# Optimization experiments

Measured on AMD Instinct MI355X. Metric: run time of the kernel, lower is better.

The kernel has to match this reference:

```python
import jax, jax.numpy as jnp
import numpy as np

# Dims (match init_kwargs)
T = 1024      # num_tokens
H = 1024      # hidden_size
F = 768       # inter_size (ffn dim)
E = 16        # expert_num
K = 4         # moe_k


def setup_inputs() -> dict:
    key = jax.random.key(0)
    k1, k2, k3, k4 = jax.random.split(key, 4)
    hidden_states = jax.random.normal(k1, (T, H), dtype=jnp.float32)
    gate_w = jax.random.normal(k2, (E, H), dtype=jnp.float32) * 0.02   # router Linear weight
    w1 = jax.random.normal(k3, (E, 2 * F, H), dtype=jnp.float32) * 0.02  # fused gate+up proj
    w2 = jax.random.normal(k4, (E, H, F), dtype=jnp.float32) * 0.02      # down proj
    return {"hidden_states": hidden_states, "gate_w": gate_w, "w1": w1, "w2": w2}


def reference(hidden_states, gate_w, w1, w2):
    x = hidden_states
    # Router gate (Linear, no bias), scores in fp32
    router_logits = jnp.einsum('th,eh->te', x, gate_w).astype(jnp.float32)
    probs = jax.nn.softmax(router_logits, axis=-1)
    # Top-k expert selection + renormalize (has_moe_norm=True)
    topk_weights, topk_ids = jax.lax.top_k(probs, K)            # [T,K]
    topk_weights = topk_weights / jnp.sum(topk_weights, axis=-1, keepdims=True)
    # Combine weights per (token, expert): [T,E]
    combine = jnp.sum(jax.nn.one_hot(topk_ids, E, dtype=topk_weights.dtype)
                      * topk_weights[..., None], axis=1)
    # Expert FFN with SiGLU (SwiGLU), computed densely over experts then combined
    h = jnp.einsum('th,efh->etf', x, w1)                         # [E,T,2F]
    gate, up = h[:, :, :F], h[:, :, F:]
    act = jax.nn.silu(gate) * up                                 # [E,T,F]
    expert_out = jnp.einsum('etf,ehf->eth', act, w2)             # [E,T,H]
    out = jnp.einsum('te,eth->th', combine, expert_out)
    return out.astype(hidden_states.dtype)
```

## Files before the change

### kernel.cpp

```cpp
#include <hip/hip_runtime.h>
#include <hip/hip_bf16.h>

#define T_TOK 1024
#define H_DIM 1024
#define F_DIM 768
#define E_NUM 16
#define TOPK  4

#define BM 64
#define BN 64
#define BK 32
#define LDSS 40

typedef __attribute__((ext_vector_type(8))) short bf16x8;
typedef __attribute__((ext_vector_type(4))) float f32x4;
typedef unsigned short ushort_t;

__device__ __forceinline__ ushort_t f2bf(float f) {
  __hip_bfloat16 h = __float2bfloat16(f);
  return *reinterpret_cast<ushort_t*>(&h);
}

__global__ void k_zero(float* __restrict__ out, int n, int* __restrict__ cnt) {
  int i = blockIdx.x * blockDim.x + threadIdx.x;
  if (i < E_NUM) cnt[i] = 0;
  for (; i < n; i += gridDim.x * blockDim.x) out[i] = 0.f;
}

__global__ __launch_bounds__(256) void k_cvt(const float* __restrict__ src,
                                             ushort_t* __restrict__ dst, int n8) {
  int i = blockIdx.x * blockDim.x + threadIdx.x;
  int stride = gridDim.x * blockDim.x;
  for (; i < n8; i += stride) {
    const float4* s = (const float4*)(src + (size_t)i * 8);
    float4 a = s[0], b = s[1];
    bf16x8 v;
    v[0] = (short)f2bf(a.x); v[1] = (short)f2bf(a.y); v[2] = (short)f2bf(a.z); v[3] = (short)f2bf(a.w);
    v[4] = (short)f2bf(b.x); v[5] = (short)f2bf(b.y); v[6] = (short)f2bf(b.z); v[7] = (short)f2bf(b.w);
    *(bf16x8*)(dst + (size_t)i * 8) = v;
  }
}

__global__ __launch_bounds__(256) void k_logits(
    const float* __restrict__ x, const float* __restrict__ gw,
    float* __restrict__ logits) {
  int wid = blockIdx.x * 4 + (threadIdx.x >> 6);
  int lane = threadIdx.x & 63;
  int t = wid >> 4;
  int e = wid & (E_NUM - 1);
  const float* xr = x + (size_t)t * H_DIM;
  const float* g  = gw + (size_t)e * H_DIM;
  float s = 0.f;
#pragma unroll
  for (int j = 0; j < 16; ++j) s += xr[lane + j * 64] * g[lane + j * 64];
#pragma unroll
  for (int off = 32; off >= 1; off >>= 1) s += __shfl_xor(s, off);
  if (lane == 0) logits[t * E_NUM + e] = s;
}

__global__ __launch_bounds__(256) void k_topk(
    const float* __restrict__ logits, int* __restrict__ cnt,
    int* __restrict__ topk_id, float* __restrict__ topk_w) {
  int t = blockIdx.x * blockDim.x + threadIdx.x;
  if (t >= T_TOK) return;

  float lg[E_NUM];
#pragma unroll
  for (int e = 0; e < E_NUM; ++e) lg[e] = logits[t * E_NUM + e];

  int ids[TOPK];
  float vals[TOPK];
  unsigned used = 0;
#pragma unroll
  for (int k = 0; k < TOPK; ++k) {
    float best = -3.0e38f;
    int bi = 0;
#pragma unroll
    for (int e = 0; e < E_NUM; ++e) {
      bool skip = (used >> e) & 1;
      if (!skip && lg[e] > best) { best = lg[e]; bi = e; }
    }
    used |= 1u << bi;
    ids[k] = bi;
    vals[k] = best;
  }
  float m = vals[0];
  float w[TOPK];
  float sum = 0.f;
#pragma unroll
  for (int k = 0; k < TOPK; ++k) { w[k] = __expf(vals[k] - m); sum += w[k]; }
  float inv = 1.f / sum;

#pragma unroll
  for (int k = 0; k < TOPK; ++k) {
    topk_id[t * TOPK + k] = ids[k];
    topk_w[t * TOPK + k] = w[k] * inv;
    atomicAdd(&cnt[ids[k]], 1);
  }
}

__global__ void k_scan(const int* __restrict__ cnt, int* __restrict__ offs,
                       int* __restrict__ cursor) {
  if (threadIdx.x == 0) {
    int r = 0;
    for (int e = 0; e < E_NUM; ++e) { offs[e] = r; r += cnt[e]; cursor[e] = 0; }
  }
}

__global__ void k_assign(const int* __restrict__ topk_id, const float* __restrict__ topk_w,
                         const int* __restrict__ offs, int* __restrict__ cursor,
                         int* __restrict__ slot_tok, float* __restrict__ slot_w) {
  int i = blockIdx.x * blockDim.x + threadIdx.x;
  if (i >= T_TOK * TOPK) return;
  int e = topk_id[i];
  int pos = offs[e] + atomicAdd(&cursor[e], 1);
  slot_tok[pos] = i >> 2;
  slot_w[pos] = topk_w[i];
}

template<bool PRE>
__global__ __launch_bounds__(256) void k_gemm1(
    const float* __restrict__ x, const float* __restrict__ w1,
    const ushort_t* __restrict__ xb, const ushort_t* __restrict__ w1b,
    const int* __restrict__ slot_tok, const int* __restrict__ offs,
    const int* __restrict__ cnt, __hip_bfloat16* __restrict__ act) {
  int e = blockIdx.z;
  int m0 = blockIdx.y * BM;
  int cntE = cnt[e];
  if (m0 >= cntE) return;
  int n0 = blockIdx.x * BN;
  int off = offs[e];

  __shared__ ushort_t sA[BM * LDSS];
  __shared__ ushort_t sG[BN * LDSS];
  __shared__ ushort_t sU[BN * LDSS];
  __shared__ int tok_s[BM];

  int tid = threadIdx.x;
  if (tid < BM) {
    int r = m0 + tid;
    tok_s[tid] = (r < cntE) ? slot_tok[off + r] : -1;
  }
  __syncthreads();

  int srow = tid >> 2;
  int scol = (tid & 3) * 8;
  int mytok = tok_s[srow];

  const float* aptr = x + (size_t)(mytok < 0 ? 0 : mytok) * H_DIM + scol;
  const float* gptr = w1 + ((size_t)e * 2 * F_DIM + n0 + srow) * H_DIM + scol;
  const float* uptr = gptr + (size_t)F_DIM * H_DIM;
  const ushort_t* aptrb = xb + (size_t)(mytok < 0 ? 0 : mytok) * H_DIM + scol;
  const ushort_t* gptrb = w1b + ((size_t)e * 2 * F_DIM + n0 + srow) * H_DIM + scol;
  const ushort_t* uptrb = gptrb + (size_t)F_DIM * H_DIM;

  int wave = tid >> 6;
  int lane = tid & 63;
  int wr = wave >> 1, wc = wave & 1;
  int lrow = lane & 15;
  int kgrp = lane >> 4;

  f32x4 accg[2][2] = {};
  f32x4 accu[2][2] = {};

  int aoff0 = (wr * 32 + lrow) * LDSS + kgrp * 8;
  int boff0 = (wc * 32 + lrow) * LDSS + kgrp * 8;

  for (int k0 = 0; k0 < H_DIM; k0 += BK) {
    bf16x8 va = {0, 0, 0, 0, 0, 0, 0, 0}, vg, vu;
    if constexpr (PRE) {
      if (mytok >= 0) va = *(const bf16x8*)(aptrb + k0);
      vg = *(const bf16x8*)(gptrb + k0);
      vu = *(const bf16x8*)(uptrb + k0);
    } else {
      float4 va0 = make_float4(0, 0, 0, 0), va1 = va0;
      if (mytok >= 0) {
        va0 = *(const float4*)(aptr + k0);
        va1 = *(const float4*)(aptr + k0 + 4);
      }
      float4 vg0 = *(const float4*)(gptr + k0);
      float4 vg1 = *(const float4*)(gptr + k0 + 4);
      float4 vu0 = *(const float4*)(uptr + k0);
      float4 vu1 = *(const float4*)(uptr + k0 + 4);
      va[0] = (short)f2bf(va0.x); va[1] = (short)f2bf(va0.y); va[2] = (short)f2bf(va0.z); va[3] = (short)f2bf(va0.w);
      va[4] = (short)f2bf(va1.x); va[5] = (short)f2bf(va1.y); va[6] = (short)f2bf(va1.z); va[7] = (short)f2bf(va1.w);
      vg[0] = (short)f2bf(vg0.x); vg[1] = (short)f2bf(vg0.y); vg[2] = (short)f2bf(vg0.z); vg[3] = (short)f2bf(vg0.w);
      vg[4] = (short)f2bf(vg1.x); vg[5] = (short)f2bf(vg1.y); vg[6] = (short)f2bf(vg1.z); vg[7] = (short)f2bf(vg1.w);
      vu[0] = (short)f2bf(vu0.x); vu[1] = (short)f2bf(vu0.y); vu[2] = (short)f2bf(vu0.z); vu[3] = (short)f2bf(vu0.w);
      vu[4] = (short)f2bf(vu1.x); vu[5] = (short)f2bf(vu1.y); vu[6] = (short)f2bf(vu1.z); vu[7] = (short)f2bf(vu1.w);
    }

    __syncthreads();
    *(bf16x8*)&sA[srow * LDSS + scol] = va;
    *(bf16x8*)&sG[srow * LDSS + scol] = vg;
    *(bf16x8*)&sU[srow * LDSS + scol] = vu;
    __syncthreads();

    bf16x8 af[2], gf[2], uf[2];
    af[0] = *(const bf16x8*)&sA[aoff0];
    af[1] = *(const bf16x8*)&sA[aoff0 + 16 * LDSS];
    gf[0] = *(const bf16x8*)&sG[boff0];
    gf[1] = *(const bf16x8*)&sG[boff0 + 16 * LDSS];
    uf[0] = *(const bf16x8*)&sU[boff0];
    uf[1] = *(const bf16x8*)&sU[boff0 + 16 * LDSS];
#pragma unroll
    for (int i = 0; i < 2; ++i)
#pragma unroll
      for (int j = 0; j < 2; ++j) {
        accg[i][j] = __builtin_amdgcn_mfma_f32_16x16x32_bf16(af[i], gf[j], accg[i][j], 0, 0, 0);
        accu[i][j] = __builtin_amdgcn_mfma_f32_16x16x32_bf16(af[i], uf[j], accu[i][j], 0, 0, 0);
      }
  }

#pragma unroll
  for (int i = 0; i < 2; ++i) {
#pragma unroll
    for (int r = 0; r < 4; ++r) {
      int row = wr * 32 + i * 16 + kgrp * 4 + r;
      if (m0 + row < cntE) {
        size_t gslot = (size_t)(off + m0 + row);
        __hip_bfloat16* ap = act + gslot * F_DIM + n0 + wc * 32 + lrow;
#pragma unroll
        for (int j = 0; j < 2; ++j) {
          float g = accg[i][j][r];
          float u = accu[i][j][r];
          float a = (g / (1.f + __expf(-g))) * u;
          ap[j * 16] = __float2bfloat16(a);
        }
      }
    }
  }
}

template<bool PRE>
__global__ __launch_bounds__(256) void k_gemm2(
    const __hip_bfloat16* __restrict__ act, const float* __restrict__ w2,
    const ushort_t* __restrict__ w2b,
    const int* __restrict__ slot_tok, const float* __restrict__ slot_w,
    const int* __restrict__ offs, const int* __restrict__ cnt,
    float* __restrict__ out) {
  int e = blockIdx.z;
  int m0 = blockIdx.y * BM;
  int cntE = cnt[e];
  if (m0 >= cntE) return;
  int n0 = blockIdx.x * BN;
  int off = offs[e];

  __shared__ ushort_t sA[BM * LDSS];
  __shared__ ushort_t sB[BN * LDSS];
  __shared__ int tok_s[BM];
  __shared__ float w_s[BM];

  int tid = threadIdx.x;
  if (tid < BM) {
    int r = m0 + tid;
    tok_s[tid] = (r < cntE) ? slot_tok[off + r] : 0;
    w_s[tid] = (r < cntE) ? slot_w[off + r] : 0.f;
  }
  __syncthreads();

  int srow = tid >> 2;
  int scol = (tid & 3) * 8;
  bool arow_ok = (m0 + srow) < cntE;
  const ushort_t* aptr = (const ushort_t*)act + (size_t)(off + m0 + (arow_ok ? srow : 0)) * F_DIM + scol;
  const float* bptr = w2 + ((size_t)e * H_DIM + n0 + srow) * F_DIM + scol;
  const ushort_t* bptrb = w2b + ((size_t)e * H_DIM + n0 + srow) * F_DIM + scol;

  int wave = tid >> 6;
  int lane = tid & 63;
  int wr = wave >> 1, wc = wave & 1;
  int lrow = lane & 15;
  int kgrp = lane >> 4;

  f32x4 acc[2][2] = {};

  int aoff0 = (wr * 32 + lrow) * LDSS + kgrp * 8;
  int boff0 = (wc * 32 + lrow) * LDSS + kgrp * 8;

  for (int k0 = 0; k0 < F_DIM; k0 += BK) {
    bf16x8 av = {0, 0, 0, 0, 0, 0, 0, 0}, vb;
    if (arow_ok) av = *(const bf16x8*)(aptr + k0);
    if constexpr (PRE) {
      vb = *(const bf16x8*)(bptrb + k0);
    } else {
      float4 vb0 = *(const float4*)(bptr + k0);
      float4 vb1 = *(const float4*)(bptr + k0 + 4);
      vb[0] = (short)f2bf(vb0.x); vb[1] = (short)f2bf(vb0.y); vb[2] = (short)f2bf(vb0.z); vb[3] = (short)f2bf(vb0.w);
      vb[4] = (short)f2bf(vb1.x); vb[5] = (short)f2bf(vb1.y); vb[6] = (short)f2bf(vb1.z); vb[7] = (short)f2bf(vb1.w);
    }

    __syncthreads();
    *(bf16x8*)&sA[srow * LDSS + scol] = av;
    *(bf16x8*)&sB[srow * LDSS + scol] = vb;
    __syncthreads();

    bf16x8 af[2], bf[2];
    af[0] = *(const bf16x8*)&sA[aoff0];
    af[1] = *(const bf16x8*)&sA[aoff0 + 16 * LDSS];
    bf[0] = *(const bf16x8*)&sB[boff0];
    bf[1] = *(const bf16x8*)&sB[boff0 + 16 * LDSS];
#pragma unroll
    for (int i = 0; i < 2; ++i)
#pragma unroll
      for (int j = 0; j < 2; ++j)
        acc[i][j] = __builtin_amdgcn_mfma_f32_16x16x32_bf16(af[i], bf[j], acc[i][j], 0, 0, 0);
  }

#pragma unroll
  for (int i = 0; i < 2; ++i) {
#pragma unroll
    for (int r = 0; r < 4; ++r) {
      int row = wr * 32 + i * 16 + kgrp * 4 + r;
      if (m0 + row < cntE) {
        int tok = tok_s[row];
        float wgt = w_s[row];
        float* op = out + (size_t)tok * H_DIM + n0 + wc * 32 + lrow;
#pragma unroll
        for (int j = 0; j < 2; ++j)
          atomicAdd(op + j * 16, acc[i][j][r] * wgt);
      }
    }
  }
}

extern "C" void kernel_launch(void* const* d_in, const int* in_sizes, int n_in,
                              void* d_out, int out_size, void* d_ws, size_t ws_size,
                              hipStream_t stream) {
  const float* x  = (const float*)d_in[0];
  const float* gw = (const float*)d_in[1];
  const float* w1 = (const float*)d_in[2];
  const float* w2 = (const float*)d_in[3];
  float* out = (float*)d_out;

  char* base = (char*)d_ws;
  int* cnt      = (int*)(base);
  int* cursor   = (int*)(base + 64);
  int* offs     = (int*)(base + 128);
  int* topk_id  = (int*)(base + 256);
  float* topk_w = (float*)(base + 256 + 16384);
  int* slot_tok = (int*)(base + 256 + 32768);
  float* slot_w = (float*)(base + 256 + 49152);
  float* logits = (float*)(base + 256 + 65536);
  __hip_bfloat16* act = (__hip_bfloat16*)(base + 256 + 131072);

  const size_t XB_OFF  = (size_t)8 << 20;
  const size_t W1B_OFF = XB_OFF + ((size_t)2 << 20);
  const size_t W2B_OFF = W1B_OFF + (size_t)E_NUM * 2 * F_DIM * H_DIM * 2;
  const size_t NEED    = W2B_OFF + (size_t)E_NUM * H_DIM * F_DIM * 2;
  bool pre = ws_size >= NEED;
  ushort_t* xb  = (ushort_t*)(base + XB_OFF);
  ushort_t* w1b = (ushort_t*)(base + W1B_OFF);
  ushort_t* w2b = (ushort_t*)(base + W2B_OFF);

  k_zero<<<512, 256, 0, stream>>>(out, T_TOK * H_DIM, cnt);
  if (pre) {
    k_cvt<<<2048, 256, 0, stream>>>(w1, w1b, E_NUM * 2 * F_DIM * H_DIM / 8);
    k_cvt<<<1024, 256, 0, stream>>>(w2, w2b, E_NUM * H_DIM * F_DIM / 8);
    k_cvt<<<256, 256, 0, stream>>>(x, xb, T_TOK * H_DIM / 8);
  }
  k_logits<<<T_TOK * E_NUM / 4, 256, 0, stream>>>(x, gw, logits);
  k_topk<<<(T_TOK + 255) / 256, 256, 0, stream>>>(logits, cnt, topk_id, topk_w);
  k_scan<<<1, 64, 0, stream>>>(cnt, offs, cursor);
  k_assign<<<(T_TOK * TOPK + 255) / 256, 256, 0, stream>>>(topk_id, topk_w, offs, cursor, slot_tok, slot_w);
  if (pre) {
    k_gemm1<true><<<dim3(F_DIM / BN, T_TOK / BM, E_NUM), 256, 0, stream>>>(
        x, w1, xb, w1b, slot_tok, offs, cnt, act);
    k_gemm2<true><<<dim3(H_DIM / BN, T_TOK / BM, E_NUM), 256, 0, stream>>>(
        act, w2, w2b, slot_tok, slot_w, offs, cnt, out);
  } else {
    k_gemm1<false><<<dim3(F_DIM / BN, T_TOK / BM, E_NUM), 256, 0, stream>>>(
        x, w1, xb, w1b, slot_tok, offs, cnt, act);
    k_gemm2<false><<<dim3(H_DIM / BN, T_TOK / BM, E_NUM), 256, 0, stream>>>(
        act, w2, w2b, slot_tok, slot_w, offs, cnt, out);
  }
}
```

Measured before the change: 316.2 us.

## Replace atomic scatter in down-proj with per-slot output buffer and gather combine

The down-projection GEMM now writes weighted per-slot results into a dense expert-output buffer instead of atomically adding into the output. A new combine kernel sums each token's four slot rows using a slot index recorded during assignment, which removes the separate output-zeroing pass. The three weight/input conversion launches are merged into one kernel, and the counter reset moves into the logits kernel. This trades fp32 atomics for an extra 16MB write and read, and it raises the workspace requirement for the fast path.

```diff
diff --git a/kernel.cpp b/kernel.cpp
--- a/kernel.cpp
+++ b/kernel.cpp
@@ -27,23 +27,33 @@
   for (; i < n; i += gridDim.x * blockDim.x) out[i] = 0.f;
 }
 
-__global__ __launch_bounds__(256) void k_cvt(const float* __restrict__ src,
-                                             ushort_t* __restrict__ dst, int n8) {
+__global__ __launch_bounds__(256) void k_cvt_all(
+    const float* __restrict__ w1, ushort_t* __restrict__ w1b,
+    const float* __restrict__ w2, ushort_t* __restrict__ w2b,
+    const float* __restrict__ x,  ushort_t* __restrict__ xb) {
+  const int N1 = E_NUM * 2 * F_DIM * H_DIM / 8;
+  const int N2 = E_NUM * H_DIM * F_DIM / 8;
+  const int N3 = T_TOK * H_DIM / 8;
   int i = blockIdx.x * blockDim.x + threadIdx.x;
   int stride = gridDim.x * blockDim.x;
-  for (; i < n8; i += stride) {
-    const float4* s = (const float4*)(src + (size_t)i * 8);
-    float4 a = s[0], b = s[1];
+  for (; i < N1 + N2 + N3; i += stride) {
+    const float* s; ushort_t* d; int j;
+    if (i < N1)            { s = w1; d = w1b; j = i; }
+    else if (i < N1 + N2)  { s = w2; d = w2b; j = i - N1; }
+    else                   { s = x;  d = xb;  j = i - N1 - N2; }
+    const float4* sp = (const float4*)(s + (size_t)j * 8);
+    float4 a = sp[0], b = sp[1];
     bf16x8 v;
     v[0] = (short)f2bf(a.x); v[1] = (short)f2bf(a.y); v[2] = (short)f2bf(a.z); v[3] = (short)f2bf(a.w);
     v[4] = (short)f2bf(b.x); v[5] = (short)f2bf(b.y); v[6] = (short)f2bf(b.z); v[7] = (short)f2bf(b.w);
-    *(bf16x8*)(dst + (size_t)i * 8) = v;
+    *(bf16x8*)(d + (size_t)j * 8) = v;
   }
 }
 
 __global__ __launch_bounds__(256) void k_logits(
     const float* __restrict__ x, const float* __restrict__ gw,
-    float* __restrict__ logits) {
+    float* __restrict__ logits, int* __restrict__ cnt) {
+  if (blockIdx.x == 0 && threadIdx.x < E_NUM) cnt[threadIdx.x] = 0;
   int wid = blockIdx.x * 4 + (threadIdx.x >> 6);
   int lane = threadIdx.x & 63;
   int t = wid >> 4;
@@ -109,13 +119,15 @@
 
 __global__ void k_assign(const int* __restrict__ topk_id, const float* __restrict__ topk_w,
                          const int* __restrict__ offs, int* __restrict__ cursor,
-                         int* __restrict__ slot_tok, float* __restrict__ slot_w) {
+                         int* __restrict__ slot_tok, float* __restrict__ slot_w,
+                         int* __restrict__ slot_of) {
   int i = blockIdx.x * blockDim.x + threadIdx.x;
   if (i >= T_TOK * TOPK) return;
   int e = topk_id[i];
   int pos = offs[e] + atomicAdd(&cursor[e], 1);
   slot_tok[pos] = i >> 2;
   slot_w[pos] = topk_w[i];
+  slot_of[i] = pos;
 }
 
 template<bool PRE>
@@ -232,10 +244,86 @@
   }
 }
 
-template<bool PRE>
-__global__ __launch_bounds__(256) void k_gemm2(
+__global__ __launch_bounds__(256) void k_gemm2eo(
+    const __hip_bfloat16* __restrict__ act, const ushort_t* __restrict__ w2b,
+    const float* __restrict__ slot_w,
+    const int* __restrict__ offs, const int* __restrict__ cnt,
+    float* __restrict__ eo) {
+  int e = blockIdx.z;
+  int m0 = blockIdx.y * BM;
+  int cntE = cnt[e];
+  if (m0 >= cntE) return;
+  int n0 = blockIdx.x * BN;
+  int off = offs[e];
+
+  __shared__ ushort_t sA[BM * LDSS];
+  __shared__ ushort_t sB[BN * LDSS];
+  __shared__ float w_s[BM];
+
+  int tid = threadIdx.x;
+  if (tid < BM) {
+    int r = m0 + tid;
+    w_s[tid] = (r < cntE) ? slot_w[off + r] : 0.f;
+  }
+  __syncthreads();
+
+  int srow = tid >> 2;
+  int scol = (tid & 3) * 8;
+  bool arow_ok = (m0 + srow) < cntE;
+  const ushort_t* aptr = (const ushort_t*)act + (size_t)(off + m0 + (arow_ok ? srow : 0)) * F_DIM + scol;
+  const ushort_t* bptrb = w2b + ((size_t)e * H_DIM + n0 + srow) * F_DIM + scol;
+
+  int wave = tid >> 6;
+  int lane = tid & 63;
+  int wr = wave >> 1, wc = wave & 1;
+  int lrow = lane & 15;
+  int kgrp = lane >> 4;
+
+  f32x4 acc[2][2] = {};
+
+  int aoff0 = (wr * 32 + lrow) * LDSS + kgrp * 8;
+  int boff0 = (wc * 32 + lrow) * LDSS + kgrp * 8;
+
+  for (int k0 = 0; k0 < F_DIM; k0 += BK) {
+    bf16x8 av = {0, 0, 0, 0, 0, 0, 0, 0};
+    if (arow_ok) av = *(const bf16x8*)(aptr + k0);
+    bf16x8 vb = *(const bf16x8*)(bptrb + k0);
+
+    __syncthreads();
+    *(bf16x8*)&sA[srow * LDSS + scol] = av;
+    *(bf16x8*)&sB[srow * LDSS + scol] = vb;
+    __syncthreads();
+
+    bf16x8 af[2], bf[2];
+    af[0] = *(const bf16x8*)&sA[aoff0];
+    af[1] = *(const bf16x8*)&sA[aoff0 + 16 * LDSS];
+    bf[0] = *(const bf16x8*)&sB[boff0];
+    bf[1] = *(const bf16x8*)&sB[boff0 + 16 * LDSS];
+#pragma unroll
+    for (int i = 0; i < 2; ++i)
+#pragma unroll
+      for (int j = 0; j < 2; ++j)
+        acc[i][j] = __builtin_amdgcn_mfma_f32_16x16x32_bf16(af[i], bf[j], acc[i][j], 0, 0, 0);
+  }
+
+#pragma unroll
+  for (int i = 0; i < 2; ++i) {
+#pragma unroll
+    for (int r = 0; r < 4; ++r) {
+      int row = wr * 32 + i * 16 + kgrp * 4 + r;
+      if (m0 + row < cntE) {
+        float wgt = w_s[row];
+        float* op = eo + (size_t)(off + m0 + row) * H_DIM + n0 + wc * 32 + lrow;
+#pragma unroll
+        for (int j = 0; j < 2; ++j)
+          op[j * 16] = acc[i][j][r] * wgt;
+      }
+    }
+  }
+}
+
+__global__ __launch_bounds__(256) void k_gemm2_atomic(
     const __hip_bfloat16* __restrict__ act, const float* __restrict__ w2,
-    const ushort_t* __restrict__ w2b,
     const int* __restrict__ slot_tok, const float* __restrict__ slot_w,
     const int* __restrict__ offs, const int* __restrict__ cnt,
     float* __restrict__ out) {
@@ -264,7 +352,6 @@
   bool arow_ok = (m0 + srow) < cntE;
   const ushort_t* aptr = (const ushort_t*)act + (size_t)(off + m0 + (arow_ok ? srow : 0)) * F_DIM + scol;
   const float* bptr = w2 + ((size_t)e * H_DIM + n0 + srow) * F_DIM + scol;
-  const ushort_t* bptrb = w2b + ((size_t)e * H_DIM + n0 + srow) * F_DIM + scol;
 
   int wave = tid >> 6;
   int lane = tid & 63;
@@ -280,14 +367,10 @@
   for (int k0 = 0; k0 < F_DIM; k0 += BK) {
     bf16x8 av = {0, 0, 0, 0, 0, 0, 0, 0}, vb;
     if (arow_ok) av = *(const bf16x8*)(aptr + k0);
-    if constexpr (PRE) {
-      vb = *(const bf16x8*)(bptrb + k0);
-    } else {
-      float4 vb0 = *(const float4*)(bptr + k0);
-      float4 vb1 = *(const float4*)(bptr + k0 + 4);
-      vb[0] = (short)f2bf(vb0.x); vb[1] = (short)f2bf(vb0.y); vb[2] = (short)f2bf(vb0.z); vb[3] = (short)f2bf(vb0.w);
-      vb[4] = (short)f2bf(vb1.x); vb[5] = (short)f2bf(vb1.y); vb[6] = (short)f2bf(vb1.z); vb[7] = (short)f2bf(vb1.w);
-    }
+    float4 vb0 = *(const float4*)(bptr + k0);
+    float4 vb1 = *(const float4*)(bptr + k0 + 4);
+    vb[0] = (short)f2bf(vb0.x); vb[1] = (short)f2bf(vb0.y); vb[2] = (short)f2bf(vb0.z); vb[3] = (short)f2bf(vb0.w);
+    vb[4] = (short)f2bf(vb1.x); vb[5] = (short)f2bf(vb1.y); vb[6] = (short)f2bf(vb1.z); vb[7] = (short)f2bf(vb1.w);
 
     __syncthreads();
     *(bf16x8*)&sA[srow * LDSS + scol] = av;
@@ -321,6 +404,27 @@
       }
     }
   }
+}
+
+__global__ __launch_bounds__(256) void k_combine(
+    const float* __restrict__ eo, const int* __restrict__ slot_of,
+    float* __restrict__ out) {
+  int t = blockIdx.x;
+  int h = threadIdx.x * 4;
+  int s0 = slot_of[t * TOPK + 0];
+  int s1 = slot_of[t * TOPK + 1];
+  int s2 = slot_of[t * TOPK + 2];
+  int s3 = slot_of[t * TOPK + 3];
+  float4 a = *(const float4*)(eo + (size_t)s0 * H_DIM + h);
+  float4 b = *(const float4*)(eo + (size_t)s1 * H_DIM + h);
+  float4 c = *(const float4*)(eo + (size_t)s2 * H_DIM + h);
+  float4 d = *(const float4*)(eo + (size_t)s3 * H_DIM + h);
+  float4 r;
+  r.x = ((a.x + b.x) + c.x) + d.x;
+  r.y = ((a.y + b.y) + c.y) + d.y;
+  r.z = ((a.z + b.z) + c.z) + d.z;
+  r.w = ((a.w + b.w) + c.w) + d.w;
+  *(float4*)(out + (size_t)t * H_DIM + h) = r;
 }
 
 extern "C" void kernel_launch(void* const* d_in, const int* in_sizes, int n_in,
@@ -342,35 +446,41 @@
   float* slot_w = (float*)(base + 256 + 49152);
   float* logits = (float*)(base + 256 + 65536);
   __hip_bfloat16* act = (__hip_bfloat16*)(base + 256 + 131072);
+  int* slot_of  = (int*)(base + ((size_t)7 << 20));
 
   const size_t XB_OFF  = (size_t)8 << 20;
   const size_t W1B_OFF = XB_OFF + ((size_t)2 << 20);
   const size_t W2B_OFF = W1B_OFF + (size_t)E_NUM * 2 * F_DIM * H_DIM * 2;
-  const size_t NEED    = W2B_OFF + (size_t)E_NUM * H_DIM * F_DIM * 2;
+  const size_t EO_OFF  = (size_t)86 << 20;
+  const size_t NEED    = EO_OFF + (size_t)T_TOK * TOPK * H_DIM * 4;
   bool pre = ws_size >= NEED;
   ushort_t* xb  = (ushort_t*)(base + XB_OFF);
   ushort_t* w1b = (ushort_t*)(base + W1B_OFF);
   ushort_t* w2b = (ushort_t*)(base + W2B_OFF);
-
-  k_zero<<<512, 256, 0, stream>>>(out, T_TOK * H_DIM, cnt);
+  float* eo     = (float*)(base + EO_OFF);
+
   if (pre) {
-    k_cvt<<<2048, 256, 0, stream>>>(w1, w1b, E_NUM * 2 * F_DIM * H_DIM / 8);
-    k_cvt<<<1024, 256, 0, stream>>>(w2, w2b, E_NUM * H_DIM * F_DIM / 8);
-    k_cvt<<<256, 256, 0, stream>>>(x, xb, T_TOK * H_DIM / 8);
-  }
-  k_logits<<<T_TOK * E_NUM / 4, 256, 0, stream>>>(x, gw, logits);
-  k_topk<<<(T_TOK + 255) / 256, 256, 0, stream>>>(logits, cnt, topk_id, topk_w);
-  k_scan<<<1, 64, 0, stream>>>(cnt, offs, cursor);
-  k_assign<<<(T_TOK * TOPK + 255) / 256, 256, 0, stream>>>(topk_id, topk_w, offs, cursor, slot_tok, slot_w);
-  if (pre) {
+    k_cvt_all<<<2048, 256, 0, stream>>>(w1, w1b, w2, w2b, x, xb);
+    k_logits<<<T_TOK * E_NUM / 4, 256, 0, stream>>>(x, gw, logits, cnt);
+    k_topk<<<(T_TOK + 255) / 256, 256, 0, stream>>>(logits, cnt, topk_id, topk_w);
+    k_scan<<<1, 64, 0, stream>>>(cnt, offs, cursor);
+    k_assign<<<(T_TOK * TOPK + 255) / 256, 256, 0, stream>>>(
+        topk_id, topk_w, offs, cursor, slot_tok, slot_w, slot_of);
     k_gemm1<true><<<dim3(F_DIM / BN, T_TOK / BM, E_NUM), 256, 0, stream>>>(
         x, w1, xb, w1b, slot_tok, offs, cnt, act);
-    k_gemm2<true><<<dim3(H_DIM / BN, T_TOK / BM, E_NUM), 256, 0, stream>>>(
-        act, w2, w2b, slot_tok, slot_w, offs, cnt, out);
+    k_gemm2eo<<<dim3(H_DIM / BN, T_TOK / BM, E_NUM), 256, 0, stream>>>(
+        act, w2b, slot_w, offs, cnt, eo);
+    k_combine<<<T_TOK, 256, 0, stream>>>(eo, slot_of, out);
   } else {
+    k_zero<<<512, 256, 0, stream>>>(out, T_TOK * H_DIM, cnt);
+    k_logits<<<T_TOK * E_NUM / 4, 256, 0, stream>>>(x, gw, logits, cnt);
+    k_topk<<<(T_TOK + 255) / 256, 256, 0, stream>>>(logits, cnt, topk_id, topk_w);
+    k_scan<<<1, 64, 0, stream>>>(cnt, offs, cursor);
+    k_assign<<<(T_TOK * TOPK + 255) / 256, 256, 0, stream>>>(
+        topk_id, topk_w, offs, cursor, slot_tok, slot_w, slot_of);
     k_gemm1<false><<<dim3(F_DIM / BN, T_TOK / BM, E_NUM), 256, 0, stream>>>(
         x, w1, xb, w1b, slot_tok, offs, cnt, act);
-    k_gemm2<false><<<dim3(H_DIM / BN, T_TOK / BM, E_NUM), 256, 0, stream>>>(
-        act, w2, w2b, slot_tok, slot_w, offs, cnt, out);
-  }
-}
+    k_gemm2_atomic<<<dim3(H_DIM / BN, T_TOK / BM, E_NUM), 256, 0, stream>>>(
+        act, w2, slot_tok, slot_w, offs, cnt, out);
+  }
+}
```

After: 314.3 us. Within noise of the previous version (-0.6%).
